# Optimization experiments

Measured on AMD Instinct MI355X. Metric: run time of the kernel, lower is better.

## Reference

```python
import jax, jax.numpy as jnp
import numpy as np

B, TE, TD = 16, 400, 64
E, H = 256, 512
H2 = 2 * H  # 1024
V = 32000


def setup_inputs():
    key = jax.random.key(0)
    k = jax.random.split(key, 16)
    s = 0.05
    return {
        "encoder_inputs": jax.random.randint(k[0], (B, TE), 0, V),
        "decoder_inputs": jax.random.randint(k[1], (B, TD), 0, V),
        "ext_oov_sizes": jax.random.randint(k[2], (B,), 0, 10),
        "enc_idxes_on_ext_voc": jax.random.randint(k[3], (B, TE), 0, V),
        "h0": jnp.zeros((2, B, H), jnp.float32),
        "c0": jnp.zeros((2, B, H), jnp.float32),
        "emb": jax.random.normal(k[4], (V, E)) * 0.1,
        "Wih_f": jax.random.normal(k[5], (4 * H, E)) * s,
        "Whh_f": jax.random.normal(k[6], (4 * H, H)) * s,
        "b_f": jnp.zeros((4 * H,), jnp.float32),
        "Wih_b": jax.random.normal(k[7], (4 * H, E)) * s,
        "Whh_b": jax.random.normal(k[8], (4 * H, H)) * s,
        "b_b": jnp.zeros((4 * H,), jnp.float32),
        "Wih_d": jax.random.normal(k[9], (4 * H2, E + 2 * H2)) * s,
        "Whh_d": jax.random.normal(k[10], (4 * H2, H2)) * s,
        "b_d": jnp.zeros((4 * H2,), jnp.float32),
        "W_ea": jax.random.normal(k[11], (H2, H2)) * 0.006,
        "W_da": jax.random.normal(k[12], (H2, H2)) * 0.006,
        "W_v": jax.random.normal(k[13], (V, 3 * H2)) * s,
        "b_v": jnp.zeros((V,), jnp.float32),
    }


def lstm_cell(x, h, c, Wih, Whh, b):
    z = x @ Wih.T + h @ Whh.T + b
    i, f, g, o = jnp.split(z, 4, axis=-1)
    i, f, o = jax.nn.sigmoid(i), jax.nn.sigmoid(f), jax.nn.sigmoid(o)
    c2 = f * c + i * jnp.tanh(g)
    return o * jnp.tanh(c2), c2


def run_lstm(xs, h0, c0, Wih, Whh, b):
    # xs: [T, B, E]
    def step(carry, x):
        h, c = lstm_cell(x, carry[0], carry[1], Wih, Whh, b)
        return (h, c), h
    (h, c), hs = jax.lax.scan(step, (h0, c0), xs)
    return hs, h, c


def _forward(emb, Wih_f, Whh_f, b_f, Wih_b, Whh_b, b_b, Wih_d, Whh_d, b_d,
             W_ea, W_da, W_v, b_v, h0, c0, encoder_inputs, decoder_inputs):
    xs = emb[encoder_inputs].transpose(1, 0, 2)  # [TE, B, E]
    hs_f, hf, cf = run_lstm(xs, h0[0], c0[0], Wih_f, Whh_f, b_f)
    hs_b, hb, cb = run_lstm(xs[::-1], h0[1], c0[1], Wih_b, Whh_b, b_b)
    enc_out = jnp.concatenate([hs_f, hs_b[::-1]], axis=-1).transpose(1, 0, 2)  # [B, TE, 2H]
    h = jnp.concatenate([hf, hb], axis=-1)  # [B, 2H] (torch reshape of bi-dir last hidden)
    c = jnp.concatenate([cf, cb], axis=-1)
    dec_emb = emb[decoder_inputs].transpose(1, 0, 2)  # [TD, B, E]

    def step(carry, xs_t):
        h, c, accum, buf = carry
        i, emb_t = xs_t
        # intra-temporal encoder attention: exp scores normalized by past accumulation
        scores = jnp.einsum('bd,btd->bt', h @ W_ea, enc_out)  # [B, TE]
        exp_s = jnp.exp(scores)
        denom = jnp.where(i == 0, jnp.ones_like(accum), accum)
        ep = exp_s / denom
        attn = ep / jnp.sum(ep, axis=-1, keepdims=True)
        ctx_e = jnp.einsum('bt,btd->bd', attn, enc_out)
        # intra-decoder attention over previously produced hidden states (masked)
        dsc = jnp.einsum('bd,tbd->bt', h @ W_da, buf)  # [B, TD]
        dsc = jnp.where((jnp.arange(TD) < i)[None, :], dsc, -1e30)
        dw = jnp.where(i == 0, 0.0, jax.nn.softmax(dsc, axis=-1))
        ctx_d = jnp.einsum('bt,tbd->bd', dw, buf)
        x = jnp.concatenate([emb_t, ctx_e, ctx_d], axis=-1)  # [B, E+4H]
        h2, c2 = lstm_cell(x, h, c, Wih_d, Whh_d, b_d)
        buf2 = buf.at[i].set(h2)
        feat = jnp.concatenate([h2, ctx_e, ctx_d], axis=-1)  # [B, 6H]
        logd = jax.nn.log_softmax(feat @ W_v.T + b_v, axis=-1)
        return (h2, c2, accum + exp_s, buf2), logd

    carry0 = (h, c, jnp.zeros((B, TE), h.dtype), jnp.zeros((TD, B, H2), h.dtype))
    (h, c, _, _), logds = jax.lax.scan(step, carry0, (jnp.arange(TD), dec_emb))
    return logds.transpose(1, 0, 2), h[None], c[None]


def reference(encoder_inputs, decoder_inputs, ext_oov_sizes, enc_idxes_on_ext_voc,
              h0, c0, emb, Wih_f, Whh_f, b_f, Wih_b, Whh_b, b_b,
              Wih_d, Whh_d, b_d, W_ea, W_da, W_v, b_v):
    # ext_oov_sizes / enc_idxes_on_ext_voc are unused by forward (as in the torch source)
    return _forward(emb, Wih_f, Whh_f, b_f, Wih_b, Whh_b, b_b, Wih_d, Whh_d, b_d,
                    W_ea, W_da, W_v, b_v, h0, c0, encoder_inputs, decoder_inputs)
```

## Files before the change

### kernel.cpp

```cpp
#include <hip/hip_runtime.h>
#include <math.h>

#define B_  16
#define TE_ 400
#define TD_ 64
#define E_  256
#define H_  512
#define H2_ 1024
#define V_  32000
#define KE_ 768

typedef __attribute__((ext_vector_type(4))) float f32x4;
typedef __attribute__((ext_vector_type(8))) short s16x8;
typedef __attribute__((ext_vector_type(8))) unsigned short u16x8;
typedef __attribute__((ext_vector_type(4))) unsigned short u16x4;

__device__ __forceinline__ float bf2f(unsigned short u){
  union { unsigned int i; float f; } v; v.i = ((unsigned int)u) << 16; return v.f;
}
__device__ __forceinline__ unsigned short f2bf(float f){
  union { float f; unsigned int i; } v; v.f = f;
  return (unsigned short)((v.i + 0x7fffu + ((v.i >> 16) & 1u)) >> 16);
}
__device__ __forceinline__ float sigmoidf_(float x){ return 1.f/(1.f + expf(-x)); }

__device__ __forceinline__ void gl_lds16(const void* gsrc, void* ldst){
  __builtin_amdgcn_global_load_lds(
      (const __attribute__((address_space(1))) unsigned int*)gsrc,
      (__attribute__((address_space(3))) unsigned int*)ldst, 16, 0, 0);
}

__device__ __forceinline__ void fast_bar(unsigned* obj, unsigned nwg, unsigned widx, unsigned epoch){
  __syncthreads();
  if (threadIdx.x == 0){
    __threadfence();
    __hip_atomic_fetch_add(&obj[(widx & 7u)*32], 1u, __ATOMIC_RELAXED, __HIP_MEMORY_SCOPE_AGENT);
    if (widx == 0){
      for(;;){
        unsigned s = 0;
        #pragma unroll
        for (int k2 = 0; k2 < 8; ++k2)
          s += __hip_atomic_load(&obj[k2*32], __ATOMIC_RELAXED, __HIP_MEMORY_SCOPE_AGENT);
        if (s >= nwg*epoch) break;
      }
      __hip_atomic_store(&obj[256], epoch, __ATOMIC_RELEASE, __HIP_MEMORY_SCOPE_AGENT);
    } else {
      while (__hip_atomic_load(&obj[256], __ATOMIC_RELAXED, __HIP_MEMORY_SCOPE_AGENT) < epoch)
        __builtin_amdgcn_s_sleep(1);
    }
    __threadfence();
  }
  __syncthreads();
}

__global__ void k_init(unsigned* bars, float* accum){
  int gid = blockIdx.x*256 + threadIdx.x;
  if (gid < 4096) bars[gid] = 0u;
  if (gid < B_*TE_) accum[gid] = 0.f;
}

__global__ void k_gather(const float* __restrict__ emb, const int* __restrict__ idx,
                         unsigned short* __restrict__ out, int T){
  int wv = threadIdx.x >> 6, l = threadIdx.x & 63;
  int row = blockIdx.x*4 + wv;
  if (row >= T*B_) return;
  int t = row >> 4, b = row & 15;
  int tok = idx[b*T + t];
  float4 v = *(const float4*)(emb + (size_t)tok*E_ + l*4);
  u16x4 o; o[0]=f2bf(v.x); o[1]=f2bf(v.y); o[2]=f2bf(v.z); o[3]=f2bf(v.w);
  *(u16x4*)(out + (size_t)row*E_ + l*4) = o;
}

__global__ void k_transpose_bf(const float* __restrict__ s, unsigned short* __restrict__ d){
  __shared__ float tile[32][33];
  int tx = threadIdx.x & 31, ty = threadIdx.x >> 5;
  int d0 = blockIdx.x*32, j0 = blockIdx.y*32;
  for (int yy = 0; yy < 32; yy += 8)
    tile[ty+yy][tx] = s[(size_t)(d0+ty+yy)*H2_ + j0 + tx];
  __syncthreads();
  for (int yy = 0; yy < 32; yy += 8)
    d[(size_t)(j0+ty+yy)*H2_ + d0 + tx] = f2bf(tile[tx][ty+yy]);
}

__global__ void k_prep_enc(const float* __restrict__ Wih_f, const float* __restrict__ Whh_f,
                           const float* __restrict__ Wih_b, const float* __restrict__ Whh_b,
                           unsigned short* __restrict__ Wenc){
  int it = blockIdx.x*256 + threadIdx.x;
  int dir = it / (2048*96); int rem = it % (2048*96);
  int pr = rem / 96; int kc = rem % 96; int k0 = kc*8;
  int g = pr >> 6, r = pr & 63, gate = r >> 4, ul = r & 15;
  int orig = gate*H_ + g*16 + ul;
  const float* Wih = dir ? Wih_b : Wih_f;
  const float* Whh = dir ? Whh_b : Whh_f;
  u16x8 o;
  #pragma unroll
  for (int e = 0; e < 8; ++e){
    int k = k0 + e;
    float v = (k < E_) ? Wih[(size_t)orig*E_ + k] : Whh[(size_t)orig*H_ + (k - E_)];
    o[e] = f2bf(v);
  }
  *(u16x8*)(Wenc + ((size_t)dir*2048 + pr)*KE_ + k0) = o;
}

__global__ void k_prep_dec(const float* __restrict__ Wih_d, const float* __restrict__ Whh_d,
                           unsigned short* __restrict__ Wd){
  int it = blockIdx.x*256 + threadIdx.x;
  int g = it / (26*64*16); int rem = it % (26*64*16);
  int kblk = rem / (64*16); int rem2 = rem % (64*16);
  int row = rem2 >> 4; int k8 = rem2 & 15;
  int gate = row >> 4, ul = row & 15;
  int orig = gate*H2_ + g*16 + ul;
  int kbase = kblk*128 + k8*8;
  u16x8 o;
  #pragma unroll
  for (int e = 0; e < 8; ++e){
    int k = kbase + e;
    float v = (k < 2304) ? Wih_d[(size_t)orig*2304 + k] : Whh_d[(size_t)orig*H2_ + (k-2304)];
    o[e] = f2bf(v);
  }
  size_t byteoff = (size_t)g*425984 + (size_t)kblk*16384 + (size_t)(row*256 + ((k8*16) ^ ((row&7)<<4)));
  *(u16x8*)((char*)Wd + byteoff) = o;
}

__global__ void __launch_bounds__(256, 1) k_encoder(
    const unsigned short* __restrict__ xs,
    const unsigned short* __restrict__ Wenc,
    const float* __restrict__ b_f, const float* __restrict__ b_b,
    const float* __restrict__ h0, const float* __restrict__ c0,
    unsigned short* __restrict__ enc_out,
    unsigned short* __restrict__ hbuf,
    float* __restrict__ h0dec, float* __restrict__ c0dec,
    unsigned* __restrict__ bars)
{
  extern __shared__ char smem[];
  unsigned short* Wt = (unsigned short*)smem;
  unsigned short* At = Wt + 64*776;
// ... 4 lines not shown
  int wv = tid >> 6, l = tid & 63;
  unsigned* bobj = bars + dir*512;
  {
    const unsigned short* Wsrc = Wenc + ((size_t)dir*2048 + g*64)*KE_;
    int r = tid >> 2, s = tid & 3;
    for (int c = 0; c < 24; ++c)
      *(u16x8*)(Wt + r*776 + s*192 + c*8) = *(const u16x8*)(Wsrc + (size_t)r*KE_ + s*192 + c*8);
  }
  const float* bias = dir ? b_b : b_f;
  int bb = tid >> 4, ul = tid & 15;
  float creg = c0[((size_t)dir*16 + bb)*H_ + g*16 + ul];
  int kchunk = (l >> 4) * 8;
  float bia = bias[wv*H_ + g*16 + (l&15)];
  f32x4 bias4 = { bia, bia, bia, bia };
  f32x4 zero4 = { 0.f, 0.f, 0.f, 0.f };
  __syncthreads();
  for (int t = 0; t < TE_; ++t){
    int tg = dir ? (TE_-1 - t) : t;
    {
      int r = tid >> 4, s = tid & 15;
      *(u16x8*)(At + r*776 + s*16)     = *(const u16x8*)(xs + ((size_t)tg*16 + r)*E_ + s*16);
      *(u16x8*)(At + r*776 + s*16 + 8) = *(const u16x8*)(xs + ((size_t)tg*16 + r)*E_ + s*16 + 8);
      if (t == 0){
        for (int e = 0; e < 32; ++e)
          At[r*776 + 256 + s*32 + e] = f2bf(h0[((size_t)dir*16 + r)*H_ + s*32 + e]);
      } else {
        const unsigned short* hsrc = hbuf + ((size_t)dir*2 + (t&1))*(16*H_) + r*H_ + s*32;
        for (int c = 0; c < 4; ++c)
          *(u16x8*)(At + r*776 + 256 + s*32 + c*8) = *(const u16x8*)(hsrc + c*8);
      }
    }
    __syncthreads();
    f32x4 acc0 = bias4, acc1 = zero4;
    const unsigned short* brow = Wt + (wv*16 + (l&15))*776 + kchunk;
    const unsigned short* ap   = At + (l&15)*776 + kchunk;
    #pragma unroll
    for (int ks = 0; ks < 24; ++ks){
      s16x8 afr = *(const s16x8*)(ap + ks*32);
      s16x8 bfr = *(const s16x8*)(brow + ks*32);
      if (ks & 1) acc1 = __builtin_amdgcn_mfma_f32_16x16x32_bf16(afr, bfr, acc1, 0, 0, 0);
      else        acc0 = __builtin_amdgcn_mfma_f32_16x16x32_bf16(afr, bfr, acc0, 0, 0, 0);
    }
    f32x4 acc = acc0 + acc1;
    #pragma unroll
    for (int j = 0; j < 4; ++j)
      zl[wv*256 + ((l>>4)*4 + j)*16 + (l&15)] = acc[j];
    __syncthreads();
// ... 1 lines not shown
    float zf = zl[1*256 + bb*16 + ul];
    float zg = zl[2*256 + bb*16 + ul];
    float zo = zl[3*256 + bb*16 + ul];
    float iv = sigmoidf_(zi), fv = sigmoidf_(zf), gv = tanhf(zg), ov = sigmoidf_(zo);
    float cc = fv*creg + iv*gv;
    float hh = ov * tanhf(cc);
    creg = cc;
    int u = g*16 + ul;
    unsigned short hb = f2bf(hh);
    hbuf[((size_t)dir*2 + ((t+1)&1))*(16*H_) + bb*H_ + u] = hb;
    enc_out[((size_t)bb*TE_ + tg)*H2_ + dir*H_ + u] = hb;
    if (t == TE_-1){
      h0dec[(size_t)bb*H2_ + dir*H_ + u] = hh;
      c0dec[(size_t)bb*H2_ + dir*H_ + u] = cc;
    }
    fast_bar(bobj, 32, (unsigned)g, (unsigned)(t+1));
  }
}

__global__ void k_dec_init(const float* __restrict__ h0dec, unsigned short* __restrict__ hreg){
  int gid = blockIdx.x*256 + threadIdx.x;
  if (gid < 16384) hreg[gid] = f2bf(h0dec[gid]);
}

__global__ void __launch_bounds__(256, 2) k_penc(
    const unsigned short* __restrict__ enc,
    const float* __restrict__ Wea,
    unsigned short* __restrict__ P)
{
  __shared__ unsigned short Ab[128*72];
  __shared__ unsigned short Bt[128*72];
// ... 49 lines not shown
  }
  #pragma unroll
  for (int fj=0;fj<4;++fj){
    int col = n0 + wc*64 + fj*16 + (l&15);
    #pragma unroll
    for (int fi=0;fi<4;++fi){
      #pragma unroll
      for (int j=0;j<4;++j){
        int row = m0 + wr*64 + fi*16 + (l>>4)*4 + j;
        P[(size_t)row*1024 + col] = f2bf(acc[fi][fj][j]);
      }
    }
  }
}

__device__ __forceinline__ void s4_issue(const char* gblk, char* Bb, int wv, int l, int kblk, int buf){
  const char* gsrc = gblk + (size_t)kblk*16384 + wv*4096 + (size_t)l*16;
  char* lb = Bb + buf*16384 + wv*4096;
  #pragma unroll
  for (int qq = 0; qq < 4; ++qq)
    gl_lds16(gsrc + qq*1024, lb + qq*1024);
}

__global__ void __launch_bounds__(256, 1) k_decoder(
  const unsigned short* __restrict__ dec_emb,
  const unsigned short* __restrict__ Wd,
  const float* __restrict__ b_d,
  const unsigned short* __restrict__ WdaT,
  const unsigned short* __restrict__ enc_out,
  const unsigned short* __restrict__ Penc,
  const float* __restrict__ c0dec,
  unsigned short* __restrict__ hreg,
  unsigned short* __restrict__ xbuf,
  float* __restrict__ q,
  float* __restrict__ accum,
  float* __restrict__ pctx,
  float* __restrict__ psum,
  float* __restrict__ bufh,
  unsigned short* __restrict__ Av,
  float* __restrict__ outHC,
  unsigned* __restrict__ bars)
{
  extern __shared__ char smem[];
  int tid = threadIdx.x, w = blockIdx.x;
  int wv = tid >> 6, l = tid & 63;
  unsigned* objA = bars + 1024;
  unsigned* objB = bars + 1536;
  unsigned* objC = bars + 2048;

  unsigned short* At = (unsigned short*)smem;
  char*  Bb = smem + 106752;
  float* zl = (float*)(smem + 155904);
  unsigned short* Ah = (unsigned short*)smem;
  unsigned short* Wq = Ah + 16*1032;
  float* zq = (float*)(Wq + 16*1032);
  float* dscL = (float*)(smem + 155904);
  unsigned short* encL = (unsigned short*)smem;
  float* epL = (float*)(smem + 102400);

  int eb = 0, ec = 0;
  if (w >= 64){ eb = (w-64) >> 3; ec = (w-64) & 7; }
  bool isL = (w < 64);

  if (w >= 64){
    for (int rr = 0; rr < 50; ++rr){
      const unsigned short* src = enc_out + ((size_t)eb*TE_ + ec*50 + rr)*H2_;
      *(u16x4*)(encL + rr*1024 + tid*4) = *(const u16x4*)(src + tid*4);
    }
    __syncthreads();
  }
  float creg = 0.f;
  int bb = tid >> 4, ul = tid & 15;

  for (int i = 0; i < TD_; ++i){
    if (isL){
      int r = tid >> 4, s = tid & 15;
      const unsigned short* hsrc = hreg + (i&1)*16384 + r*H2_ + s*64;
      for (int c = 0; c < 8; ++c)
        *(u16x8*)(Ah + r*1032 + s*64 + c*8) = *(const u16x8*)(hsrc + c*8);
      __syncthreads();
      const unsigned short* Wsrc = WdaT + (size_t)w*16*H2_;
      for (int c = 0; c < 8; ++c)
        *(u16x8*)(Wq + r*1032 + s*64 + c*8) = *(const u16x8*)(Wsrc + (size_t)r*H2_ + s*64 + c*8);
      __syncthreads();
      f32x4 acc = {0.f,0.f,0.f,0.f};
      const unsigned short* ap = Ah + (l&15)*1032 + wv*256 + (l>>4)*8;
      const unsigned short* bp = Wq + (l&15)*1032 + wv*256 + (l>>4)*8;
      #pragma unroll
      for (int ks = 0; ks < 8; ++ks){
        s16x8 afr = *(const s16x8*)(ap + ks*32);
        s16x8 bfr = *(const s16x8*)(bp + ks*32);
        acc = __builtin_amdgcn_mfma_f32_16x16x32_bf16(afr, bfr, acc, 0,0,0);
      }
      #pragma unroll
      for (int j = 0; j < 4; ++j)
        zq[wv*256 + (l&15)*16 + (l>>4)*4 + j] = acc[j];
      __syncthreads();
      float qv = zq[0*256 + (tid&15)*16 + (tid>>4)] + zq[1*256 + (tid&15)*16 + (tid>>4)]
               + zq[2*256 + (tid&15)*16 + (tid>>4)] + zq[3*256 + (tid&15)*16 + (tid>>4)];
      q[(size_t)(tid>>4)*H2_ + w*16 + (tid&15)] = qv;
    } else {
      const unsigned short* hb_ = hreg + (i&1)*16384 + eb*H2_ + l*16;
      u16x8 hv0 = *(const u16x8*)hb_;
      u16x8 hv1 = *(const u16x8*)(hb_ + 8);
      float hf[16];
      #pragma unroll
      for (int c = 0; c < 8; ++c){ hf[c] = bf2f(hv0[c]); hf[8+c] = bf2f(hv1[c]); }
      for (int rr = wv; rr < 50; rr += 4){
        const unsigned short* pr = Penc + ((size_t)(eb*TE_ + ec*50 + rr))*H2_ + l*16;
        u16x8 p0 = *(const u16x8*)pr;
        u16x8 p1 = *(const u16x8*)(pr + 8);
        float sc = 0.f;
        #pragma unroll
        for (int c = 0; c < 8; ++c) sc += hf[c]*bf2f(p0[c]);
        #pragma unroll
// ... 14 lines not shown
      for (int rr = 0; rr < 50; ++rr) tot += epL[rr];
      float a0=0.f,a1=0.f,a2=0.f,a3=0.f;
      for (int rr = 0; rr < 50; ++rr){
        float wgt = epL[rr];
        u16x4 ev = *(const u16x4*)(encL + rr*1024 + tid*4);
        a0 += wgt*bf2f(ev[0]); a1 += wgt*bf2f(ev[1]); a2 += wgt*bf2f(ev[2]); a3 += wgt*bf2f(ev[3]);
      }
      int slot = w - 64;
      float4 o4; o4.x=a0; o4.y=a1; o4.z=a2; o4.w=a3;
      *(float4*)(pctx + (size_t)slot*1024 + tid*4) = o4;
      if (tid == 0) psum[slot] = tot;
      __syncthreads();
    }
    fast_bar(objA, 192, (unsigned)w, (unsigned)(i+1));

    if (w < 16){
      int b = w;
      if (i == 0){
        int col = tid*4;
        u16x4 z4 = {0,0,0,0};
        *(u16x4*)(xbuf + (size_t)b*2048 + 1024 + col) = z4;
        *(u16x4*)(Av + ((size_t)b*TD_ + i)*3072 + 2048 + col) = z4;
      } else {
        const float* qsrc = q + (size_t)b*H2_ + l*16;
        float4 q0 = *(const float4*)(qsrc);
        float4 q1 = *(const float4*)(qsrc+4);
        float4 q2 = *(const float4*)(qsrc+8);
        float4 q3 = *(const float4*)(qsrc+12);
        for (int tp = wv; tp < i; tp += 4){
          const float* br = bufh + ((size_t)tp*16 + b)*H2_ + l*16;
          float4 b0 = *(const float4*)(br);
          float4 b1 = *(const float4*)(br+4);
          float4 b2 = *(const float4*)(br+8);
          float4 b3 = *(const float4*)(br+12);
          float sc = q0.x*b0.x + q0.y*b0.y + q0.z*b0.z + q0.w*b0.w
                   + q1.x*b1.x + q1.y*b1.y + q1.z*b1.z + q1.w*b1.w
                   + q2.x*b2.x + q2.y*b2.y + q2.z*b2.z + q2.w*b2.w
                   + q3.x*b3.x + q3.y*b3.y + q3.z*b3.z + q3.w*b3.w;
          #pragma unroll
          for (int o = 1; o < 64; o <<= 1) sc += __shfl_xor(sc, o);
          if (l == 0) dscL[tp] = sc;
        }
        __syncthreads();
        float scv = (l < i) ? dscL[l] : -1e30f;
        float m = scv;
        #pragma unroll
        for (int o = 1; o < 64; o <<= 1) m = fmaxf(m, __shfl_xor(m, o));
        float e = (l < i) ? expf(scv - m) : 0.f;
        float ssum = e;
        #pragma unroll
        for (int o = 1; o < 64; o <<= 1) ssum += __shfl_xor(ssum, o);
        float wgt = e / ssum;
        int col = wv*256 + l*4;
        float c0_=0.f,c1_=0.f,c2_=0.f,c3_=0.f;
        for (int tp = 0; tp < i; ++tp){
          float wt = __shfl(wgt, tp);
          const float* br = bufh + ((size_t)tp*16 + b)*H2_ + col;
          float4 bv = *(const float4*)br;
          c0_ += wt*bv.x; c1_ += wt*bv.y; c2_ += wt*bv.z; c3_ += wt*bv.w;
        }
        u16x4 o4; o4[0]=f2bf(c0_); o4[1]=f2bf(c1_); o4[2]=f2bf(c2_); o4[3]=f2bf(c3_);
        *(u16x4*)(xbuf + (size_t)b*2048 + 1024 + col) = o4;
        *(u16x4*)(Av + ((size_t)b*TD_ + i)*3072 + 2048 + col) = o4;
      }
    } else if (w < 32){
      int b = w - 16;
      float sx=0.f, sy=0.f, sz=0.f, sw=0.f, pst=0.f;
      for (int c = 0; c < 8; ++c){
        float4 v = *(const float4*)(pctx + (size_t)(b*8+c)*1024 + tid*4);
        sx += v.x; sy += v.y; sz += v.z; sw += v.w;
        pst += psum[b*8+c];
      }
      float inv = 1.f/pst;
      u16x4 o; o[0]=f2bf(sx*inv); o[1]=f2bf(sy*inv); o[2]=f2bf(sz*inv); o[3]=f2bf(sw*inv);
      *(u16x4*)(xbuf + (size_t)b*2048 + tid*4) = o;
      *(u16x4*)(Av + ((size_t)b*TD_ + i)*3072 + 1024 + tid*4) = o;
    }
    fast_bar(objB, 192, (unsigned)w, (unsigned)(i+1));

    if (isL){
      int r = tid >> 4, s = tid & 15;
      *(u16x8*)(At + r*3336 + s*16)     = *(const u16x8*)(dec_emb + ((size_t)i*16 + r)*E_ + s*16);
      *(u16x8*)(At + r*3336 + s*16 + 8) = *(const u16x8*)(dec_emb + ((size_t)i*16 + r)*E_ + s*16 + 8);
      for (int c = 0; c < 16; ++c)
        *(u16x8*)(At + r*3336 + 256 + s*128 + c*8) = *(const u16x8*)(xbuf + (size_t)r*2048 + s*128 + c*8);
      for (int c = 0; c < 8; ++c)
        *(u16x8*)(At + r*3336 + 2304 + s*64 + c*8) = *(const u16x8*)(hreg + (i&1)*16384 + (size_t)r*H2_ + s*64 + c*8);
      __syncthreads();
      float bia = b_d[wv*H2_ + w*16 + (l&15)];
      f32x4 acc0 = { bia, bia, bia, bia };
      f32x4 acc1 = { 0.f, 0.f, 0.f, 0.f };
      const char* gblk = (const char*)Wd + (size_t)w*425984;
      int r2 = wv*16 + (l&15);
      s4_issue(gblk, Bb, wv, l, 0, 0);
      s4_issue(gblk, Bb, wv, l, 1, 1);
      for (int kblk = 0; kblk < 26; ++kblk){
        int buf = kblk % 3;
        if (kblk + 2 < 26) s4_issue(gblk, Bb, wv, l, kblk+2, (kblk+2)%3);
        if (kblk < 24)       asm volatile("s_waitcnt vmcnt(8)" ::: "memory");
        else if (kblk == 24) asm volatile("s_waitcnt vmcnt(4)" ::: "memory");
        else                 asm volatile("s_waitcnt vmcnt(0)" ::: "memory");
        const unsigned short* ap = At + (l&15)*3336 + kblk*128 + (l>>4)*8;
        const char* Bbase = Bb + buf*16384;
        #pragma unroll
        for (int ks = 0; ks < 4; ++ks){
          int k8 = ks*4 + (l>>4);
          int bby = r2*256 + ((k8*16) ^ ((r2&7)<<4));
          s16x8 afr = *(const s16x8*)(ap + ks*32);
          s16x8 bfr = *(const s16x8*)(Bbase + bby);
          if (ks & 1) acc1 = __builtin_amdgcn_mfma_f32_16x16x32_bf16(afr, bfr, acc1, 0,0,0);
          else        acc0 = __builtin_amdgcn_mfma_f32_16x16x32_bf16(afr, bfr, acc0, 0,0,0);
        }
      }
      f32x4 acc = acc0 + acc1;
      #pragma unroll
      for (int j = 0; j < 4; ++j)
        zl[wv*256 + ((l>>4)*4+j)*16 + (l&15)] = acc[j];
      __syncthreads();
      float zi = zl[0*256 + bb*16 + ul];
      float zf = zl[1*256 + bb*16 + ul];
      float zg = zl[2*256 + bb*16 + ul];
      float zo = zl[3*256 + bb*16 + ul];
      if (i == 0) creg = c0dec[(size_t)bb*H2_ + w*16 + ul];
      float iv = sigmoidf_(zi), fv = sigmoidf_(zf), gv = tanhf(zg), ov = sigmoidf_(zo);
      float cc = fv*creg + iv*gv;
      float hh = ov*tanhf(cc);
      creg = cc;
      int u = w*16 + ul;
      hreg[((i+1)&1)*16384 + (size_t)bb*H2_ + u] = f2bf(hh);
      Av[((size_t)bb*TD_ + i)*3072 + u] = f2bf(hh);
      bufh[((size_t)i*16 + bb)*H2_ + u] = hh;
      if (i == TD_-1){
        outHC[(size_t)bb*H2_ + u] = hh;
        outHC[16384 + (size_t)bb*H2_ + u] = cc;
      }
    }
    fast_bar(objC, 192, (unsigned)w, (unsigned)(i+1));
  }
}

__global__ void __launch_bounds__(256, 2) k_vocab_gemm(
    const unsigned short* __restrict__ Av,
    const float* __restrict__ Wv,
    const float* __restrict__ bv,
    float* __restrict__ out)
{
// ... 107 lines not shown
  const float* Whh_d= (const float*)d_in[14];
  const float* b_d  = (const float*)d_in[15];
  const float* W_ea = (const float*)d_in[16];
  const float* W_da = (const float*)d_in[17];
  const float* W_v  = (const float*)d_in[18];
  const float* b_v  = (const float*)d_in[19];
  float* out = (float*)d_out;
  char* ws = (char*)d_ws;

  size_t o_bars   = 0;
  size_t o_accum  = 16384;
  size_t o_q      = o_accum + 25600;
  size_t o_xs     = o_q + 65536;
  size_t o_decemb = o_xs + (size_t)6400*256*2;
  size_t o_Wenc   = o_decemb + (size_t)1024*256*2;
  size_t o_Wd     = o_Wenc + (size_t)2*2048*768*2;
  size_t o_WdaT   = o_Wd + (size_t)64*425984;
  size_t o_enc    = o_WdaT + (size_t)1024*1024*2;
  size_t o_Penc   = o_enc + (size_t)16*400*1024*2;
  size_t o_hbuf   = o_Penc + (size_t)16*400*1024*2;
  size_t o_h0dec  = o_hbuf + (size_t)2*2*16*512*2;
  size_t o_c0dec  = o_h0dec + (size_t)16*1024*4;
  size_t o_hreg   = o_c0dec + (size_t)16*1024*4;
  size_t o_xbuf   = o_hreg + (size_t)2*16*1024*2;
  size_t o_pctx   = o_xbuf + (size_t)16*2048*2;
  size_t o_psum   = o_pctx + (size_t)128*1024*4;
  size_t o_bufh   = o_psum + 512;
  size_t o_Av     = o_bufh + (size_t)64*16*1024*4;

  unsigned* bars        = (unsigned*)(ws + o_bars);
  float* accum          = (float*)(ws + o_accum);
  float* q              = (float*)(ws + o_q);
  unsigned short* xs    = (unsigned short*)(ws + o_xs);
  unsigned short* decemb= (unsigned short*)(ws + o_decemb);
  unsigned short* Wenc  = (unsigned short*)(ws + o_Wenc);
  unsigned short* Wd    = (unsigned short*)(ws + o_Wd);
  unsigned short* WdaT  = (unsigned short*)(ws + o_WdaT);
  unsigned short* encO  = (unsigned short*)(ws + o_enc);
  unsigned short* Penc  = (unsigned short*)(ws + o_Penc);
  unsigned short* hbuf  = (unsigned short*)(ws + o_hbuf);
  float* h0dec          = (float*)(ws + o_h0dec);
  float* c0dec          = (float*)(ws + o_c0dec);
  unsigned short* hreg  = (unsigned short*)(ws + o_hreg);
  unsigned short* xbuf  = (unsigned short*)(ws + o_xbuf);
  float* pctx           = (float*)(ws + o_pctx);
  float* psum           = (float*)(ws + o_psum);
  float* bufh           = (float*)(ws + o_bufh);
  unsigned short* Av    = (unsigned short*)(ws + o_Av);

  hipFuncSetAttribute((const void*)k_encoder, hipFuncAttributeMaxDynamicSharedMemorySize, 131072);
  hipFuncSetAttribute((const void*)k_decoder, hipFuncAttributeMaxDynamicSharedMemorySize, 160000);

  k_init<<<26, 256, 0, stream>>>(bars, accum);
  k_gather<<<1600, 256, 0, stream>>>(emb, enc_in, xs, TE_);
  k_gather<<<256, 256, 0, stream>>>(emb, dec_in, decemb, TD_);
  k_prep_enc<<<1536, 256, 0, stream>>>(Wih_f, Whh_f, Wih_b, Whh_b, Wenc);
  k_prep_dec<<<6656, 256, 0, stream>>>(Wih_d, Whh_d, Wd);
  dim3 tg(32, 32, 1);
  k_transpose_bf<<<tg, 256, 0, stream>>>(W_da, WdaT);
  k_encoder<<<64, 256, 128512, stream>>>(xs, Wenc, b_f, b_b, h0, c0, encO, hbuf, h0dec, c0dec, bars);
  k_penc<<<400, 256, 0, stream>>>(encO, W_ea, Penc);
  k_dec_init<<<64, 256, 0, stream>>>(h0dec, hreg);
  k_decoder<<<192, 256, 160000, stream>>>(decemb, Wd, b_d, WdaT, encO, Penc, c0dec,
                                          hreg, xbuf, q, accum, pctx, psum, bufh, Av,
                                          out + (size_t)32768000, bars);
  k_vocab_gemm<<<2048, 256, 0, stream>>>(Av, W_v, b_v, out);
  k_logsoftmax<<<1024, 256, 0, stream>>>(out);
}
```

Baseline: 6.192 ms.

## Split decoder gate GEMM, precompute embedding gates, overlap encoder loads with barrier

The decoder's input-embedding contribution to the LSTM gates (plus bias) is now precomputed for all steps in one batched GEMM. The per-step recurrent Whh part is fused with the W_da query projection and issued before the first barrier, leaving only the context part after the second barrier, with its weights prefetched early. The encoder barrier is split into arrive and wait so the next token's input load overlaps the wait. The decoder history buffer is stored as bf16 instead of fp32 to halve its traffic. Risks include the extra precompute kernels, new weight layouts and the precision loss in stored hidden states.

```diff
diff --git a/kernel.cpp b/kernel.cpp
--- a/kernel.cpp
+++ b/kernel.cpp
@@ -30,11 +30,15 @@
       (__attribute__((address_space(3))) unsigned int*)ldst, 16, 0, 0);
 }
 
-__device__ __forceinline__ void fast_bar(unsigned* obj, unsigned nwg, unsigned widx, unsigned epoch){
+__device__ __forceinline__ void bar_arrive(unsigned* obj, unsigned widx){
   __syncthreads();
   if (threadIdx.x == 0){
     __threadfence();
     __hip_atomic_fetch_add(&obj[(widx & 7u)*32], 1u, __ATOMIC_RELAXED, __HIP_MEMORY_SCOPE_AGENT);
+  }
+}
+__device__ __forceinline__ void bar_wait(unsigned* obj, unsigned nwg, unsigned widx, unsigned epoch){
+  if (threadIdx.x == 0){
     if (widx == 0){
       for(;;){
         unsigned s = 0;
@@ -51,6 +55,10 @@
     __threadfence();
   }
   __syncthreads();
+}
+__device__ __forceinline__ void fast_bar(unsigned* obj, unsigned nwg, unsigned widx, unsigned epoch){
+  bar_arrive(obj, widx);
+  bar_wait(obj, nwg, widx, epoch);
 }
 
 __global__ void k_init(unsigned* bars, float* accum){
@@ -69,17 +77,6 @@
   float4 v = *(const float4*)(emb + (size_t)tok*E_ + l*4);
   u16x4 o; o[0]=f2bf(v.x); o[1]=f2bf(v.y); o[2]=f2bf(v.z); o[3]=f2bf(v.w);
   *(u16x4*)(out + (size_t)row*E_ + l*4) = o;
-}
-
-__global__ void k_transpose_bf(const float* __restrict__ s, unsigned short* __restrict__ d){
-  __shared__ float tile[32][33];
-  int tx = threadIdx.x & 31, ty = threadIdx.x >> 5;
-  int d0 = blockIdx.x*32, j0 = blockIdx.y*32;
-  for (int yy = 0; yy < 32; yy += 8)
-    tile[ty+yy][tx] = s[(size_t)(d0+ty+yy)*H2_ + j0 + tx];
-  __syncthreads();
-  for (int yy = 0; yy < 32; yy += 8)
-    d[(size_t)(j0+ty+yy)*H2_ + d0 + tx] = f2bf(tile[tx][ty+yy]);
 }
 
 __global__ void k_prep_enc(const float* __restrict__ Wih_f, const float* __restrict__ Whh_f,
@@ -102,24 +99,124 @@
   *(u16x8*)(Wenc + ((size_t)dir*2048 + pr)*KE_ + k0) = o;
 }
 
-__global__ void k_prep_dec(const float* __restrict__ Wih_d, const float* __restrict__ Whh_d,
-                           unsigned short* __restrict__ Wd){
+__global__ void k_prep_whext(const float* __restrict__ Whh_d, const float* __restrict__ W_da,
+                             char* __restrict__ WhExt){
   int it = blockIdx.x*256 + threadIdx.x;
-  int g = it / (26*64*16); int rem = it % (26*64*16);
-  int kblk = rem / (64*16); int rem2 = rem % (64*16);
+  if (it < 524288){
+    int g = it >> 13; int rem = it & 8191;
+    int kblk = rem >> 10; int rem2 = rem & 1023;
+    int row = rem2 >> 4; int k8 = rem2 & 15;
+    int gate = row >> 4, ul = row & 15;
+    int orig = gate*H2_ + g*16 + ul;
+    u16x8 o;
+    #pragma unroll
+    for (int e = 0; e < 8; ++e)
+      o[e] = f2bf(Whh_d[(size_t)orig*H2_ + kblk*128 + k8*8 + e]);
+    size_t off = (size_t)g*163840 + (size_t)kblk*20480 + (size_t)(row*256 + ((k8*16) ^ ((row&7)<<4)));
+    *(u16x8*)(WhExt + off) = o;
+  } else if (it < 655360){
+    int qi = it - 524288;
+    int g = qi >> 11; int rem = qi & 2047;
+    int kblk = rem >> 8; int c2 = rem & 255;
+    int wv = c2 >> 6, rr = (c2 >> 2) & 15, c = c2 & 3;
+    u16x8 o;
+    #pragma unroll
+    for (int e = 0; e < 8; ++e)
+      o[e] = f2bf(W_da[(size_t)(g*16 + rr)*H2_ + kblk*128 + wv*32 + c*8 + e]);
+    size_t off = (size_t)g*163840 + (size_t)kblk*20480 + 16384 + (size_t)(wv*1024 + rr*64 + ((c*16) ^ ((rr&7)<<4)));
+    *(u16x8*)(WhExt + off) = o;
+  }
+}
+
+__global__ void k_prep_ctx(const float* __restrict__ Wih_d, char* __restrict__ CtxW){
+  int it = blockIdx.x*256 + threadIdx.x;
+  int g = it >> 14; int rem = it & 16383;
+  int kblk = rem >> 10; int rem2 = rem & 1023;
   int row = rem2 >> 4; int k8 = rem2 & 15;
   int gate = row >> 4, ul = row & 15;
   int orig = gate*H2_ + g*16 + ul;
-  int kbase = kblk*128 + k8*8;
+  int k = 256 + kblk*128 + k8*8;
   u16x8 o;
   #pragma unroll
-  for (int e = 0; e < 8; ++e){
-    int k = kbase + e;
-    float v = (k < 2304) ? Wih_d[(size_t)orig*2304 + k] : Whh_d[(size_t)orig*H2_ + (k-2304)];
-    o[e] = f2bf(v);
-  }
-  size_t byteoff = (size_t)g*425984 + (size_t)kblk*16384 + (size_t)(row*256 + ((k8*16) ^ ((row&7)<<4)));
-  *(u16x8*)((char*)Wd + byteoff) = o;
+  for (int e = 0; e < 8; ++e)
+    o[e] = f2bf(Wih_d[(size_t)orig*2304 + k + e]);
+  size_t off = (size_t)g*262144 + (size_t)kblk*16384 + (size_t)(row*256 + ((k8*16) ^ ((row&7)<<4)));
+  *(u16x8*)(CtxW + off) = o;
+}
+
+__global__ void k_prep_wihemb(const float* __restrict__ Wih_d, unsigned short* __restrict__ Wemb){
+  int it = blockIdx.x*256 + threadIdx.x;
+  int p = it >> 5; int k0 = (it & 31)*8;
+  int g = p >> 6, gate = (p >> 4) & 3, ul = p & 15;
+  int orig = gate*H2_ + g*16 + ul;
+  u16x8 o;
+  #pragma unroll
+  for (int e = 0; e < 8; ++e)
+    o[e] = f2bf(Wih_d[(size_t)orig*2304 + k0 + e]);
+  *(u16x8*)(Wemb + (size_t)p*256 + k0) = o;
+}
+
+__global__ void __launch_bounds__(256, 2) k_zinit(
+    const unsigned short* __restrict__ A,
+    const unsigned short* __restrict__ Bw,
+    const float* __restrict__ bd,
+    float* __restrict__ Cz)
+{
+  __shared__ unsigned short Ab[128*72];
+  __shared__ unsigned short Bt[128*72];
+  int p = blockIdx.x;
+  int mt = p >> 5, nt = p & 31;
+  int m0 = mt*128, n0 = nt*128;
+  int tid = threadIdx.x, wvv = tid>>6, l = tid&63;
+  int wr = wvv>>1, wc = wvv&1;
+  f32x4 zero4 = {0.f,0.f,0.f,0.f};
+  f32x4 acc[4][4];
+  #pragma unroll
+  for (int a=0;a<4;++a){
+    #pragma unroll
+    for (int b=0;b<4;++b) acc[a][b] = zero4;
+  }
+  for (int k0 = 0; k0 < 256; k0 += 64){
+    #pragma unroll
+    for (int qq = 0; qq < 4; ++qq){
+      int idx8 = (tid + qq*256)*8;
+      int r = idx8 >> 6, k = idx8 & 63;
+      *(u16x8*)(Ab + r*72 + k) = *(const u16x8*)(A + (size_t)(m0+r)*256 + k0 + k);
+      *(u16x8*)(Bt + r*72 + k) = *(const u16x8*)(Bw + (size_t)(n0+r)*256 + k0 + k);
+    }
+    __syncthreads();
+    #pragma unroll
+    for (int ks = 0; ks < 2; ++ks){
+      s16x8 af[4], bf[4];
+      #pragma unroll
+      for (int fi=0;fi<4;++fi)
+        af[fi] = *(const s16x8*)(Ab + (wr*64+fi*16+(l&15))*72 + ks*32 + (l>>4)*8);
+      #pragma unroll
+      for (int fj=0;fj<4;++fj)
+        bf[fj] = *(const s16x8*)(Bt + (wc*64+fj*16+(l&15))*72 + ks*32 + (l>>4)*8);
+      #pragma unroll
+      for (int fi=0;fi<4;++fi){
+        #pragma unroll
+        for (int fj=0;fj<4;++fj)
+          acc[fi][fj] = __builtin_amdgcn_mfma_f32_16x16x32_bf16(af[fi], bf[fj], acc[fi][fj], 0,0,0);
+      }
+    }
+    __syncthreads();
+  }
+  #pragma unroll
+  for (int fj=0;fj<4;++fj){
+    int col = n0 + wc*64 + fj*16 + (l&15);
+    int orig = ((col>>4)&3)*H2_ + (col>>6)*16 + (col&15);
+    float bias = bd[orig];
+    #pragma unroll
+    for (int fi=0;fi<4;++fi){
+      #pragma unroll
+      for (int j=0;j<4;++j){
+        int row = m0 + wr*64 + fi*16 + (l>>4)*4 + j;
+        Cz[(size_t)row*4096 + col] = acc[fi][fj][j] + bias;
+      }
+    }
+  }
 }
 
 __global__ void __launch_bounds__(256, 1) k_encoder(
@@ -154,23 +251,17 @@
   float bia = bias[wv*H_ + g*16 + (l&15)];
   f32x4 bias4 = { bia, bia, bia, bia };
   f32x4 zero4 = { 0.f, 0.f, 0.f, 0.f };
+  {
+    int r = tid >> 4, s = tid & 15;
+    int tg0 = dir ? (TE_-1) : 0;
+    *(u16x8*)(At + r*776 + s*16)     = *(const u16x8*)(xs + ((size_t)tg0*16 + r)*E_ + s*16);
+    *(u16x8*)(At + r*776 + s*16 + 8) = *(const u16x8*)(xs + ((size_t)tg0*16 + r)*E_ + s*16 + 8);
+    for (int e = 0; e < 32; ++e)
+      At[r*776 + 256 + s*32 + e] = f2bf(h0[((size_t)dir*16 + r)*H_ + s*32 + e]);
+  }
   __syncthreads();
   for (int t = 0; t < TE_; ++t){
     int tg = dir ? (TE_-1 - t) : t;
-    {
-      int r = tid >> 4, s = tid & 15;
-      *(u16x8*)(At + r*776 + s*16)     = *(const u16x8*)(xs + ((size_t)tg*16 + r)*E_ + s*16);
-      *(u16x8*)(At + r*776 + s*16 + 8) = *(const u16x8*)(xs + ((size_t)tg*16 + r)*E_ + s*16 + 8);
-      if (t == 0){
-        for (int e = 0; e < 32; ++e)
-          At[r*776 + 256 + s*32 + e] = f2bf(h0[((size_t)dir*16 + r)*H_ + s*32 + e]);
-      } else {
-        const unsigned short* hsrc = hbuf + ((size_t)dir*2 + (t&1))*(16*H_) + r*H_ + s*32;
-        for (int c = 0; c < 4; ++c)
-          *(u16x8*)(At + r*776 + 256 + s*32 + c*8) = *(const u16x8*)(hsrc + c*8);
-      }
-    }
-    __syncthreads();
     f32x4 acc0 = bias4, acc1 = zero4;
     const unsigned short* brow = Wt + (wv*16 + (l&15))*776 + kchunk;
     const unsigned short* ap   = At + (l&15)*776 + kchunk;
@@ -202,7 +293,21 @@
       h0dec[(size_t)bb*H2_ + dir*H_ + u] = hh;
       c0dec[(size_t)bb*H2_ + dir*H_ + u] = cc;
     }
-    fast_bar(bobj, 32, (unsigned)g, (unsigned)(t+1));
+    bar_arrive(bobj, (unsigned)g);
+    if (t+1 < TE_){
+      int r = tid >> 4, s = tid & 15;
+      int tg2 = dir ? (TE_-2 - t) : (t+1);
+      *(u16x8*)(At + r*776 + s*16)     = *(const u16x8*)(xs + ((size_t)tg2*16 + r)*E_ + s*16);
+      *(u16x8*)(At + r*776 + s*16 + 8) = *(const u16x8*)(xs + ((size_t)tg2*16 + r)*E_ + s*16 + 8);
+    }
+    bar_wait(bobj, 32, (unsigned)g, (unsigned)(t+1));
+    if (t+1 < TE_){
+      int r = tid >> 4, s = tid & 15;
+      const unsigned short* hsrc = hbuf + ((size_t)dir*2 + ((t+1)&1))*(16*H_) + r*H_ + s*32;
+      for (int c = 0; c < 4; ++c)
+        *(u16x8*)(At + r*776 + 256 + s*32 + c*8) = *(const u16x8*)(hsrc + c*8);
+    }
+    __syncthreads();
   }
 }
 
@@ -282,21 +387,28 @@
   }
 }
 
-__device__ __forceinline__ void s4_issue(const char* gblk, char* Bb, int wv, int l, int kblk, int buf){
-  const char* gsrc = gblk + (size_t)kblk*16384 + wv*4096 + (size_t)l*16;
-  char* lb = Bb + buf*16384 + wv*4096;
-  #pragma unroll
-  for (int qq = 0; qq < 4; ++qq)
-    gl_lds16(gsrc + qq*1024, lb + qq*1024);
+__device__ __forceinline__ void issueA(const char* gA, char* Bb, int wv, int l, int kblk, int buf){
+  const char* gsrc = gA + (size_t)kblk*20480;
+  char* lb = Bb + buf*20480;
+  #pragma unroll
+  for (int q = 0; q < 4; ++q)
+    gl_lds16(gsrc + wv*4096 + q*1024 + (size_t)l*16, lb + wv*4096 + q*1024);
+  gl_lds16(gsrc + 16384 + wv*1024 + (size_t)l*16, lb + 16384 + wv*1024);
+}
+__device__ __forceinline__ void issueC(const char* gC, char* Bb, int wv, int l, int kblk, int buf){
+  const char* gsrc = gC + (size_t)kblk*16384;
+  char* lb = Bb + buf*20480;
+  #pragma unroll
+  for (int q = 0; q < 4; ++q)
+    gl_lds16(gsrc + wv*4096 + q*1024 + (size_t)l*16, lb + wv*4096 + q*1024);
 }
 
 __global__ void __launch_bounds__(256, 1) k_decoder(
-  const unsigned short* __restrict__ dec_emb,
-  const unsigned short* __restrict__ Wd,
-  const float* __restrict__ b_d,
-  const unsigned short* __restrict__ WdaT,
+  const char* __restrict__ WhExt,
+  const char* __restrict__ CtxW,
+  const float* __restrict__ zinit,
+  const unsigned short* __restrict__ Penc,
   const unsigned short* __restrict__ enc_out,
-  const unsigned short* __restrict__ Penc,
   const float* __restrict__ c0dec,
   unsigned short* __restrict__ hreg,
   unsigned short* __restrict__ xbuf,
@@ -304,7 +416,7 @@
   float* __restrict__ accum,
   float* __restrict__ pctx,
   float* __restrict__ psum,
-  float* __restrict__ bufh,
+  unsigned short* __restrict__ bufh,
   unsigned short* __restrict__ Av,
   float* __restrict__ outHC,
   unsigned* __restrict__ bars)
@@ -316,19 +428,18 @@
   unsigned* objB = bars + 1536;
   unsigned* objC = bars + 2048;
 
-  unsigned short* At = (unsigned short*)smem;
-  char*  Bb = smem + 106752;
-  float* zl = (float*)(smem + 155904);
-  unsigned short* Ah = (unsigned short*)smem;
-  unsigned short* Wq = Ah + 16*1032;
-  float* zq = (float*)(Wq + 16*1032);
-  float* dscL = (float*)(smem + 155904);
+  unsigned short* Atc = (unsigned short*)smem;
+  unsigned short* Ah  = (unsigned short*)smem;
+  char*  Bb = smem + 66560;
+  float* zl = (float*)(smem + 148480);
+  float* zq = (float*)(smem + 152576);
   unsigned short* encL = (unsigned short*)smem;
-  float* epL = (float*)(smem + 102400);
-
+  float* epL  = (float*)(smem + 102400);
+  float* dscL = (float*)(smem + 103424);
+
+  bool isL = (w < 64);
   int eb = 0, ec = 0;
   if (w >= 64){ eb = (w-64) >> 3; ec = (w-64) & 7; }
-  bool isL = (w < 64);
 
   if (w >= 64){
     for (int rr = 0; rr < 50; ++rr){
@@ -339,34 +450,60 @@
   }
   float creg = 0.f;
   int bb = tid >> 4, ul = tid & 15;
+  const char* gA = (const char*)WhExt + (size_t)w*163840;
+  const char* gC = (const char*)CtxW + (size_t)w*262144;
+
+  f32x4 acc0, acc1;
 
   for (int i = 0; i < TD_; ++i){
     if (isL){
-      int r = tid >> 4, s = tid & 15;
-      const unsigned short* hsrc = hreg + (i&1)*16384 + r*H2_ + s*64;
-      for (int c = 0; c < 8; ++c)
-        *(u16x8*)(Ah + r*1032 + s*64 + c*8) = *(const u16x8*)(hsrc + c*8);
+      issueA(gA, Bb, wv, l, 0, 0);
+      issueA(gA, Bb, wv, l, 1, 1);
+      {
+        int r = tid >> 4, s = tid & 15;
+        const unsigned short* hsrc = hreg + (i&1)*16384 + r*H2_ + s*64;
+        for (int c = 0; c < 8; ++c)
+          *(u16x8*)(Ah + r*1032 + s*64 + c*8) = *(const u16x8*)(hsrc + c*8);
+      }
       __syncthreads();
-      const unsigned short* Wsrc = WdaT + (size_t)w*16*H2_;
-      for (int c = 0; c < 8; ++c)
-        *(u16x8*)(Wq + r*1032 + s*64 + c*8) = *(const u16x8*)(Wsrc + (size_t)r*H2_ + s*64 + c*8);
+      {
+        const float* zsrc = zinit + ((size_t)i*16 + (l>>4)*4)*4096 + w*64 + wv*16 + (l&15);
+        f32x4 a; a[0]=zsrc[0]; a[1]=zsrc[4096]; a[2]=zsrc[8192]; a[3]=zsrc[12288];
+        acc0 = a;
+        f32x4 z4 = {0.f,0.f,0.f,0.f};
+        acc1 = z4;
+      }
+      f32x4 accq = {0.f,0.f,0.f,0.f};
+      int swz = ((l&7)<<4);
+      for (int kblk = 0; kblk < 8; ++kblk){
+        int buf = kblk % 3;
+        if (kblk + 2 < 8) issueA(gA, Bb, wv, l, kblk+2, (kblk+2)%3);
+        if (kblk < 6)       asm volatile("s_waitcnt vmcnt(10)" ::: "memory");
+        else if (kblk == 6) asm volatile("s_waitcnt vmcnt(5)" ::: "memory");
+        else                asm volatile("s_waitcnt vmcnt(0)" ::: "memory");
+        const unsigned short* ap = Ah + (l&15)*1032 + kblk*128 + (l>>4)*8;
+        const char* Bz = Bb + buf*20480 + wv*4096;
+        #pragma unroll
+        for (int ks = 0; ks < 4; ++ks){
+          int k8 = ks*4 + (l>>4);
+          s16x8 afr = *(const s16x8*)(ap + ks*32);
+          s16x8 bfr = *(const s16x8*)(Bz + (l&15)*256 + ((k8*16) ^ swz));
+          if (ks & 1) acc1 = __builtin_amdgcn_mfma_f32_16x16x32_bf16(afr, bfr, acc1, 0,0,0);
+          else        acc0 = __builtin_amdgcn_mfma_f32_16x16x32_bf16(afr, bfr, acc0, 0,0,0);
+        }
+        {
+          s16x8 afq = *(const s16x8*)(Ah + (l&15)*1032 + kblk*128 + wv*32 + (l>>4)*8);
+          s16x8 bfq = *(const s16x8*)(Bb + buf*20480 + 16384 + wv*1024 + (l&15)*64 + ((((l>>4)*16)) ^ swz));
+          accq = __builtin_amdgcn_mfma_f32_16x16x32_bf16(afq, bfq, accq, 0,0,0);
+        }
+      }
+      #pragma unroll
+      for (int j = 0; j < 4; ++j)
+        zq[wv*256 + ((l>>4)*4+j)*16 + (l&15)] = accq[j];
       __syncthreads();
-      f32x4 acc = {0.f,0.f,0.f,0.f};
-      const unsigned short* ap = Ah + (l&15)*1032 + wv*256 + (l>>4)*8;
-      const unsigned short* bp = Wq + (l&15)*1032 + wv*256 + (l>>4)*8;
-      #pragma unroll
-      for (int ks = 0; ks < 8; ++ks){
-        s16x8 afr = *(const s16x8*)(ap + ks*32);
-        s16x8 bfr = *(const s16x8*)(bp + ks*32);
-        acc = __builtin_amdgcn_mfma_f32_16x16x32_bf16(afr, bfr, acc, 0,0,0);
-      }
-      #pragma unroll
-      for (int j = 0; j < 4; ++j)
-        zq[wv*256 + (l&15)*16 + (l>>4)*4 + j] = acc[j];
-      __syncthreads();
-      float qv = zq[0*256 + (tid&15)*16 + (tid>>4)] + zq[1*256 + (tid&15)*16 + (tid>>4)]
-               + zq[2*256 + (tid&15)*16 + (tid>>4)] + zq[3*256 + (tid&15)*16 + (tid>>4)];
-      q[(size_t)(tid>>4)*H2_ + w*16 + (tid&15)] = qv;
+      float qv = zq[0*256 + bb*16 + ul] + zq[1*256 + bb*16 + ul]
+               + zq[2*256 + bb*16 + ul] + zq[3*256 + bb*16 + ul];
+      q[(size_t)bb*H2_ + w*16 + ul] = qv;
     } else {
       const unsigned short* hb_ = hreg + (i&1)*16384 + eb*H2_ + l*16;
       u16x8 hv0 = *(const u16x8*)hb_;
@@ -411,29 +548,30 @@
     }
     fast_bar(objA, 192, (unsigned)w, (unsigned)(i+1));
 
-    if (w < 16){
-      int b = w;
+    if (isL){
+      #pragma unroll
+      for (int j = 0; j < 4; ++j)
+        issueC(gC, Bb, wv, l, j, j);
+    } else if (w < 96){
+      int b = (w-64) >> 1, half = w & 1;
+      int col = half*512 + tid*2;
       if (i == 0){
-        int col = tid*4;
-        u16x4 z4 = {0,0,0,0};
-        *(u16x4*)(xbuf + (size_t)b*2048 + 1024 + col) = z4;
-        *(u16x4*)(Av + ((size_t)b*TD_ + i)*3072 + 2048 + col) = z4;
+        *(unsigned*)(xbuf + (size_t)b*2048 + 1024 + col) = 0u;
+        *(unsigned*)(Av + ((size_t)b*TD_ + i)*3072 + 2048 + col) = 0u;
       } else {
-        const float* qsrc = q + (size_t)b*H2_ + l*16;
-        float4 q0 = *(const float4*)(qsrc);
-        float4 q1 = *(const float4*)(qsrc+4);
-        float4 q2 = *(const float4*)(qsrc+8);
-        float4 q3 = *(const float4*)(qsrc+12);
+        const float* qp = q + (size_t)b*H2_ + l*16;
+        float4 q0 = *(const float4*)(qp);
+        float4 q1 = *(const float4*)(qp+4);
+        float4 q2 = *(const float4*)(qp+8);
+        float4 q3 = *(const float4*)(qp+12);
         for (int tp = wv; tp < i; tp += 4){
-          const float* br = bufh + ((size_t)tp*16 + b)*H2_ + l*16;
-          float4 b0 = *(const float4*)(br);
-          float4 b1 = *(const float4*)(br+4);
-          float4 b2 = *(const float4*)(br+8);
-          float4 b3 = *(const float4*)(br+12);
-          float sc = q0.x*b0.x + q0.y*b0.y + q0.z*b0.z + q0.w*b0.w
-                   + q1.x*b1.x + q1.y*b1.y + q1.z*b1.z + q1.w*b1.w
-                   + q2.x*b2.x + q2.y*b2.y + q2.z*b2.z + q2.w*b2.w
-                   + q3.x*b3.x + q3.y*b3.y + q3.z*b3.z + q3.w*b3.w;
+          const unsigned short* br = bufh + ((size_t)tp*16 + b)*H2_ + l*16;
+          u16x8 e0 = *(const u16x8*)(br);
+          u16x8 e1 = *(const u16x8*)(br + 8);
+          float sc = q0.x*bf2f(e0[0]) + q0.y*bf2f(e0[1]) + q0.z*bf2f(e0[2]) + q0.w*bf2f(e0[3])
+                   + q1.x*bf2f(e0[4]) + q1.y*bf2f(e0[5]) + q1.z*bf2f(e0[6]) + q1.w*bf2f(e0[7])
+                   + q2.x*bf2f(e1[0]) + q2.y*bf2f(e1[1]) + q2.z*bf2f(e1[2]) + q2.w*bf2f(e1[3])
+                   + q3.x*bf2f(e1[4]) + q3.y*bf2f(e1[5]) + q3.z*bf2f(e1[6]) + q3.w*bf2f(e1[7]);
           #pragma unroll
           for (int o = 1; o < 64; o <<= 1) sc += __shfl_xor(sc, o);
           if (l == 0) dscL[tp] = sc;
@@ -448,20 +586,19 @@
         #pragma unroll
         for (int o = 1; o < 64; o <<= 1) ssum += __shfl_xor(ssum, o);
         float wgt = e / ssum;
-        int col = wv*256 + l*4;
-        float c0_=0.f,c1_=0.f,c2_=0.f,c3_=0.f;
+        float c0_ = 0.f, c1_ = 0.f;
         for (int tp = 0; tp < i; ++tp){
           float wt = __shfl(wgt, tp);
-          const float* br = bufh + ((size_t)tp*16 + b)*H2_ + col;
-          float4 bv = *(const float4*)br;
-          c0_ += wt*bv.x; c1_ += wt*bv.y; c2_ += wt*bv.z; c3_ += wt*bv.w;
+          unsigned hv = *(const unsigned*)(bufh + ((size_t)tp*16 + b)*H2_ + col);
+          c0_ += wt*bf2f((unsigned short)hv);
+          c1_ += wt*bf2f((unsigned short)(hv>>16));
         }
-        u16x4 o4; o4[0]=f2bf(c0_); o4[1]=f2bf(c1_); o4[2]=f2bf(c2_); o4[3]=f2bf(c3_);
-        *(u16x4*)(xbuf + (size_t)b*2048 + 1024 + col) = o4;
-        *(u16x4*)(Av + ((size_t)b*TD_ + i)*3072 + 2048 + col) = o4;
-      }
-    } else if (w < 32){
-      int b = w - 16;
+        unsigned o2 = (unsigned)f2bf(c0_) | ((unsigned)f2bf(c1_) << 16);
+        *(unsigned*)(xbuf + (size_t)b*2048 + 1024 + col) = o2;
+        *(unsigned*)(Av + ((size_t)b*TD_ + i)*3072 + 2048 + col) = o2;
+      }
+    } else if (w < 112){
+      int b = w - 96;
       float sx=0.f, sy=0.f, sz=0.f, sw=0.f, pst=0.f;
       for (int c = 0; c < 8; ++c){
         float4 v = *(const float4*)(pctx + (size_t)(b*8+c)*1024 + tid*4);
@@ -476,38 +613,30 @@
     fast_bar(objB, 192, (unsigned)w, (unsigned)(i+1));
 
     if (isL){
-      int r = tid >> 4, s = tid & 15;
-      *(u16x8*)(At + r*3336 + s*16)     = *(const u16x8*)(dec_emb + ((size_t)i*16 + r)*E_ + s*16);
-      *(u16x8*)(At + r*3336 + s*16 + 8) = *(const u16x8*)(dec_emb + ((size_t)i*16 + r)*E_ + s*16 + 8);
-      for (int c = 0; c < 16; ++c)
-        *(u16x8*)(At + r*3336 + 256 + s*128 + c*8) = *(const u16x8*)(xbuf + (size_t)r*2048 + s*128 + c*8);
-      for (int c = 0; c < 8; ++c)
-        *(u16x8*)(At + r*3336 + 2304 + s*64 + c*8) = *(const u16x8*)(hreg + (i&1)*16384 + (size_t)r*H2_ + s*64 + c*8);
+      {
+        int r = tid >> 4, s = tid & 15;
+        for (int c = 0; c < 16; ++c)
+          *(u16x8*)(Atc + r*2056 + s*128 + c*8) = *(const u16x8*)(xbuf + (size_t)r*2048 + s*128 + c*8);
+      }
       __syncthreads();
-      float bia = b_d[wv*H2_ + w*16 + (l&15)];
-      f32x4 acc0 = { bia, bia, bia, bia };
-      f32x4 acc1 = { 0.f, 0.f, 0.f, 0.f };
-      const char* gblk = (const char*)Wd + (size_t)w*425984;
-      int r2 = wv*16 + (l&15);
-      s4_issue(gblk, Bb, wv, l, 0, 0);
-      s4_issue(gblk, Bb, wv, l, 1, 1);
-      for (int kblk = 0; kblk < 26; ++kblk){
-        int buf = kblk % 3;
-        if (kblk + 2 < 26) s4_issue(gblk, Bb, wv, l, kblk+2, (kblk+2)%3);
-        if (kblk < 24)       asm volatile("s_waitcnt vmcnt(8)" ::: "memory");
-        else if (kblk == 24) asm volatile("s_waitcnt vmcnt(4)" ::: "memory");
-        else                 asm volatile("s_waitcnt vmcnt(0)" ::: "memory");
-        const unsigned short* ap = At + (l&15)*3336 + kblk*128 + (l>>4)*8;
-        const char* Bbase = Bb + buf*16384;
+      int swz = ((l&7)<<4);
+      for (int kblk = 0; kblk < 16; ++kblk){
+        int buf = kblk & 3;
+        if (kblk >= 4 && kblk <= 12) asm volatile("s_waitcnt vmcnt(12)" ::: "memory");
+        else if (kblk == 13)         asm volatile("s_waitcnt vmcnt(8)" ::: "memory");
+        else if (kblk == 14)         asm volatile("s_waitcnt vmcnt(4)" ::: "memory");
+        else if (kblk == 15)         asm volatile("s_waitcnt vmcnt(0)" ::: "memory");
+        const unsigned short* ap = Atc + (l&15)*2056 + kblk*128 + (l>>4)*8;
+        const char* Bz = Bb + buf*20480 + wv*4096;
         #pragma unroll
         for (int ks = 0; ks < 4; ++ks){
           int k8 = ks*4 + (l>>4);
-          int bby = r2*256 + ((k8*16) ^ ((r2&7)<<4));
           s16x8 afr = *(const s16x8*)(ap + ks*32);
-          s16x8 bfr = *(const s16x8*)(Bbase + bby);
+          s16x8 bfr = *(const s16x8*)(Bz + (l&15)*256 + ((k8*16) ^ swz));
           if (ks & 1) acc1 = __builtin_amdgcn_mfma_f32_16x16x32_bf16(afr, bfr, acc1, 0,0,0);
           else        acc0 = __builtin_amdgcn_mfma_f32_16x16x32_bf16(afr, bfr, acc0, 0,0,0);
         }
+        if (kblk + 4 < 16) issueC(gC, Bb, wv, l, kblk+4, buf);
       }
       f32x4 acc = acc0 + acc1;
       #pragma unroll
@@ -524,9 +653,10 @@
       float hh = ov*tanhf(cc);
       creg = cc;
       int u = w*16 + ul;
-      hreg[((i+1)&1)*16384 + (size_t)bb*H2_ + u] = f2bf(hh);
-      Av[((size_t)bb*TD_ + i)*3072 + u] = f2bf(hh);
-      bufh[((size_t)i*16 + bb)*H2_ + u] = hh;
+      unsigned short hb2 = f2bf(hh);
+      hreg[((i+1)&1)*16384 + (size_t)bb*H2_ + u] = hb2;
+      Av[((size_t)bb*TD_ + i)*3072 + u] = hb2;
+      bufh[((size_t)i*16 + bb)*H2_ + u] = hb2;
       if (i == TD_-1){
         outHC[(size_t)bb*H2_ + u] = hh;
         outHC[16384 + (size_t)bb*H2_ + u] = cc;
@@ -664,9 +794,11 @@
   size_t o_xs     = o_q + 65536;
   size_t o_decemb = o_xs + (size_t)6400*256*2;
   size_t o_Wenc   = o_decemb + (size_t)1024*256*2;
-  size_t o_Wd     = o_Wenc + (size_t)2*2048*768*2;
-  size_t o_WdaT   = o_Wd + (size_t)64*425984;
-  size_t o_enc    = o_WdaT + (size_t)1024*1024*2;
+  size_t o_WhExt  = o_Wenc + (size_t)2*2048*768*2;
+  size_t o_CtxW   = o_WhExt + (size_t)64*163840;
+  size_t o_Wemb   = o_CtxW + (size_t)64*262144;
+  size_t o_zinit  = o_Wemb + (size_t)4096*256*2;
+  size_t o_enc    = o_zinit + (size_t)1024*4096*4;
   size_t o_Penc   = o_enc + (size_t)16*400*1024*2;
   size_t o_hbuf   = o_Penc + (size_t)16*400*1024*2;
   size_t o_h0dec  = o_hbuf + (size_t)2*2*16*512*2;
@@ -676,7 +808,7 @@
   size_t o_pctx   = o_xbuf + (size_t)16*2048*2;
   size_t o_psum   = o_pctx + (size_t)128*1024*4;
   size_t o_bufh   = o_psum + 512;
-  size_t o_Av     = o_bufh + (size_t)64*16*1024*4;
+  size_t o_Av     = o_bufh + (size_t)64*16*1024*2;
 
   unsigned* bars        = (unsigned*)(ws + o_bars);
   float* accum          = (float*)(ws + o_accum);
@@ -684,8 +816,10 @@
   unsigned short* xs    = (unsigned short*)(ws + o_xs);
   unsigned short* decemb= (unsigned short*)(ws + o_decemb);
   unsigned short* Wenc  = (unsigned short*)(ws + o_Wenc);
-  unsigned short* Wd    = (unsigned short*)(ws + o_Wd);
-  unsigned short* WdaT  = (unsigned short*)(ws + o_WdaT);
+  char* WhExt           = ws + o_WhExt;
+  char* CtxW            = ws + o_CtxW;
+  unsigned short* Wemb  = (unsigned short*)(ws + o_Wemb);
+  float* zinit          = (float*)(ws + o_zinit);
   unsigned short* encO  = (unsigned short*)(ws + o_enc);
   unsigned short* Penc  = (unsigned short*)(ws + o_Penc);
   unsigned short* hbuf  = (unsigned short*)(ws + o_hbuf);
@@ -695,23 +829,24 @@
   unsigned short* xbuf  = (unsigned short*)(ws + o_xbuf);
   float* pctx           = (float*)(ws + o_pctx);
   float* psum           = (float*)(ws + o_psum);
-  float* bufh           = (float*)(ws + o_bufh);
+  unsigned short* bufh  = (unsigned short*)(ws + o_bufh);
   unsigned short* Av    = (unsigned short*)(ws + o_Av);
 
   hipFuncSetAttribute((const void*)k_encoder, hipFuncAttributeMaxDynamicSharedMemorySize, 131072);
-  hipFuncSetAttribute((const void*)k_decoder, hipFuncAttributeMaxDynamicSharedMemorySize, 160000);
+  hipFuncSetAttribute((const void*)k_decoder, hipFuncAttributeMaxDynamicSharedMemorySize, 157696);
 
   k_init<<<26, 256, 0, stream>>>(bars, accum);
   k_gather<<<1600, 256, 0, stream>>>(emb, enc_in, xs, TE_);
   k_gather<<<256, 256, 0, stream>>>(emb, dec_in, decemb, TD_);
   k_prep_enc<<<1536, 256, 0, stream>>>(Wih_f, Whh_f, Wih_b, Whh_b, Wenc);
-  k_prep_dec<<<6656, 256, 0, stream>>>(Wih_d, Whh_d, Wd);
-  dim3 tg(32, 32, 1);
-  k_transpose_bf<<<tg, 256, 0, stream>>>(W_da, WdaT);
+  k_prep_whext<<<2560, 256, 0, stream>>>(Whh_d, W_da, WhExt);
+  k_prep_ctx<<<4096, 256, 0, stream>>>(Wih_d, CtxW);
+  k_prep_wihemb<<<512, 256, 0, stream>>>(Wih_d, Wemb);
+  k_zinit<<<256, 256, 0, stream>>>(decemb, Wemb, b_d, zinit);
   k_encoder<<<64, 256, 128512, stream>>>(xs, Wenc, b_f, b_b, h0, c0, encO, hbuf, h0dec, c0dec, bars);
   k_penc<<<400, 256, 0, stream>>>(encO, W_ea, Penc);
   k_dec_init<<<64, 256, 0, stream>>>(h0dec, hreg);
-  k_decoder<<<192, 256, 160000, stream>>>(decemb, Wd, b_d, WdaT, encO, Penc, c0dec,
+  k_decoder<<<192, 256, 156672, stream>>>(WhExt, CtxW, zinit, Penc, encO, c0dec,
                                           hreg, xbuf, q, accum, pctx, psum, bufh, Av,
                                           out + (size_t)32768000, bars);
   k_vocab_gemm<<<2048, 256, 0, stream>>>(Av, W_v, b_v, out);
```

Measured after the change: 6.342 ms. +2.4%, slower.
